# Kernel optimization log

Hardware: AMD Instinct MI355X
Metric: run time of the kernel (lower is better)

## Reference

```python
import jax, jax.numpy as jnp
import numpy as np

jax.config.update("jax_enable_x64", True)  # original uses torch fp64 for the reciprocal trick

# --- GenericE layout constants ---
N = 32            # NUM_POSITIONS
D = 128           # per-position feature dim
F = N * D         # flattened dim
B = 8192          # batch
NIB_A, NIB_B = 0, 1
SLOT_DIVIDEND, SLOT_DIVISOR, SLOT_REMAINDER, SLOT_QUOTIENT = 2, 3, 4, 5
OP_START, OPCODE, BASE = 64, 3, 2
S = 60.0          # DIV_SCALE
SM_S = 60.0       # SOFTMAX1_SCALE
OP_FLAT = 0 * D + OP_START + OPCODE  # flat index of opcode channel at position 0


def _build_weights():
    # ClearDivSlotsFFN: hidden_dim = 4 slots * 2 units; bake_clear_pair wiring
    cW_up = np.zeros((8, F), np.float32)
    cW_gate = np.zeros((8, F), np.float32)
    cW_down = np.zeros((F, 8), np.float32)
    for i, slot in enumerate([SLOT_DIVIDEND, SLOT_DIVISOR, SLOT_REMAINDER, SLOT_QUOTIENT]):
        h = 2 * i
        # delta[slot] = -(1/S) * relu(S*op_w) * slot_val  -> clears slot when opcode active
        cW_up[h, OP_FLAT] = S
        cW_gate[h, slot] = 1.0
        cW_down[slot, h] = -1.0 / S
        # guard unit of the pair (zero down weight, mirrors gather's guard unit)
        cW_up[h + 1, OP_FLAT] = -S
        cW_gate[h + 1, slot] = -1.0
    # GatherScalarFFN: hidden_dim = N + 1; wiring straight from the source
    H = N + 1
    gW_up = np.zeros((H, F), np.float32)
    gW_gate = np.zeros((H, F), np.float32)
    gW_down = np.zeros((F, H), np.float32)
    dst = 0 * D + SLOT_DIVIDEND
    for i in range(N):
        gW_up[i, OP_FLAT] = S
        gW_gate[i, i * D + NIB_A] = float(BASE ** i)
        gW_down[dst, i] = 1.0 / S
    gW_up[N, OP_FLAT] = -S
    gW_gate[N, dst] = -1.0
    # gW_down[dst, N] = 0.0 (explicit in source)
    return (jnp.asarray(cW_up), jnp.asarray(cW_gate), jnp.asarray(cW_down),
            jnp.asarray(gW_up), jnp.asarray(gW_gate), jnp.asarray(gW_down))


def setup_inputs() -> dict:
    key = jax.random.key(0)
    x = jax.random.uniform(key, (B, N, D), dtype=jnp.float32)
    cW_up, cW_gate, cW_down, gW_up, gW_gate, gW_down = _build_weights()
    base_powers = jnp.asarray([float(BASE ** j) for j in range(N)], dtype=jnp.float64)
    return {"x": x, "cW_up": cW_up, "cW_gate": cW_gate, "cW_down": cW_down,
            "gW_up": gW_up, "gW_gate": gW_gate, "gW_down": gW_down,
            "base_powers": base_powers}


def _ffn_delta(xf, W_up, W_gate, W_down):
    # GenericFlattenedFFN residual delta: W_down @ (relu(W_up x) * (W_gate x))
    h = jax.nn.relu(xf @ W_up.T) * (xf @ W_gate.T)   # [B, H]
    return h @ W_down.T                               # [B, F]


def reference(x, cW_up, cW_gate, cW_down, gW_up, gW_gate, gW_down, base_powers):
    Bc, Nc, Dc = x.shape
    xf = x.reshape(Bc, Nc * Dc)
    # d1 + d2: the two FFN branches (each branch's forward is x + delta, so diff is delta)
    d12 = _ffn_delta(xf, cW_up, cW_gate, cW_down) + _ffn_delta(xf, gW_up, gW_gate, gW_down)
    # d3: Softmax1 reciprocal trick in fp64 (matching torch .double())
    op_w = x[:, 0, OP_START + OPCODE]                         # [B]
    d = x[:, :Nc, NIB_B].astype(jnp.float64)                  # [B, N]
    val = jnp.maximum(d * base_powers, 0.5)
    scores = jnp.where(d > 0.5, jnp.log(val), jnp.float64(-SM_S))
    mx = scores.max(axis=-1, keepdims=True)                   # [B, 1]
    sum_ex = jnp.exp(scores - mx).sum(axis=-1)                # [B]
    recip = jnp.exp(-mx[..., 0]) / jnp.maximum(sum_ex, 1e-30)
    out = x + d12.reshape(Bc, Nc, Dc)
    return out.at[:, 0, SLOT_QUOTIENT].add(op_w * recip.astype(x.dtype))
```

## Files before the change

kernel.cpp:

```cpp
#include <hip/hip_runtime.h>
#include <math.h>


#define DDIM 128
#define FDIM 4096

__global__ __launch_bounds__(256) void div_merged_kernel(
    const float* __restrict__ x, float* __restrict__ out) {
  const long long row = blockIdx.x;
  const float* __restrict__ xr = x + row * (long long)FDIM;
  float* __restrict__ orow = out + row * (long long)FDIM;
  const int t = threadIdx.x;

  __shared__ float s_fix[4];

  if (t < 64) {
    const int lane = t;
    const bool active = lane < 32;
    double score = -60.0;
    double p = 0.0;
    if (active) {
      const double pw = (double)(1ULL << lane);
      const float va = xr[lane * DDIM + 0];
      const float vb = xr[lane * DDIM + 1];
      p = (double)va * pw;
      const double d = (double)vb;
      score = (d > 0.5) ? log(fmax(d * pw, 0.5)) : -60.0;
    }
    double mx = score;
#pragma unroll
    for (int off = 1; off < 64; off <<= 1)
      mx = fmax(mx, __shfl_xor(mx, off));
    double ex = active ? exp(score - mx) : 0.0;
#pragma unroll
    for (int off = 1; off < 64; off <<= 1) {
      ex += __shfl_xor(ex, off);
      p  += __shfl_xor(p, off);
    }
    if (lane == 0) {
      const float op    = xr[67];
      const float r60   = fmaxf(60.0f * op, 0.0f);
      const float inv60 = (float)(1.0 / 60.0);
      const double recip = exp(-mx) / fmax(ex, 1e-30);
      const float Pf = (float)p;
      const float x2 = xr[2], x3 = xr[3], x4v = xr[4], x5 = xr[5];
      const float dc2 = -((r60 * x2) * inv60);
      const float dc3 = -((r60 * x3) * inv60);
      const float dc4 = -((r60 * x4v) * inv60);
      const float dc5 = -((r60 * x5) * inv60);
      const float dg2 = (r60 * Pf) * inv60;
      s_fix[0] = x2 + (dc2 + dg2);
      s_fix[1] = x3 + dc3;
      s_fix[2] = x4v + dc4;
      s_fix[3] = (x5 + dc5) + op * (float)recip;
    }
  }
  __syncthreads();

  const float4* __restrict__ x4 = (const float4*)xr;
  float4* __restrict__ o4 = (float4*)orow;
#pragma unroll
  for (int k = 0; k < 4; ++k) {
    const int idx = k * 256 + t;
    float4 v = x4[idx];
    if (idx == 0) {
      v.z = s_fix[0];
      v.w = s_fix[1];
    } else if (idx == 1) {
      v.x = s_fix[2];
      v.y = s_fix[3];
    }
    o4[idx] = v;
  }
}

extern "C" void kernel_launch(void* const* d_in, const int* in_sizes, int n_in,
                              void* d_out, int out_size, void* d_ws, size_t ws_size,
                              hipStream_t stream) {
  const float* x = (const float*)d_in[0];
  float* out = (float*)d_out;
  const int rows = in_sizes[0] / FDIM;
  div_merged_kernel<<<rows, 256, 0, stream>>>(x, out);
}
```

Measured before the change: 244.0 us.

## Split per-row fixup into separate wave-per-row blocks, removing block barrier

The fixup work (softmax reciprocal over 32 positions and the slot updates) moves into dedicated blocks that each handle four rows, one wave per row. The bulk copy blocks no longer wait on a __syncthreads for that fixup and simply copy every float4 except the first two, which the fixup waves write. This is meant to remove the serialized fp64 reduction from the critical path of each copy block. In exchange it adds extra blocks, relies on rows being a multiple of 4, and has fixup waves rereading the row's first floats.

```diff
diff --git a/kernel.cpp b/kernel.cpp
--- a/kernel.cpp
+++ b/kernel.cpp
@@ -6,25 +6,26 @@
 #define FDIM 4096
 
 __global__ __launch_bounds__(256) void div_merged_kernel(
-    const float* __restrict__ x, float* __restrict__ out) {
-  const long long row = blockIdx.x;
-  const float* __restrict__ xr = x + row * (long long)FDIM;
-  float* __restrict__ orow = out + row * (long long)FDIM;
+    const float* __restrict__ x, float* __restrict__ out, int rows) {
+  const int bid = blockIdx.x;
   const int t = threadIdx.x;
+  const int nfix = rows >> 2;
 
-  __shared__ float s_fix[4];
+  if (bid < nfix) {
+    const int wave = t >> 6;
+    const int lane = t & 63;
+    const long long row = (long long)bid * 4 + wave;
+    const float* __restrict__ xr = x + row * (long long)FDIM;
+    float* __restrict__ orow = out + row * (long long)FDIM;
 
-  if (t < 64) {
-    const int lane = t;
     const bool active = lane < 32;
     double score = -60.0;
     double p = 0.0;
     if (active) {
+      const float2 ab = *(const float2*)(xr + lane * DDIM);
       const double pw = (double)(1ULL << lane);
-      const float va = xr[lane * DDIM + 0];
-      const float vb = xr[lane * DDIM + 1];
-      p = (double)va * pw;
-      const double d = (double)vb;
+      p = (double)ab.x * pw;
+      const double d = (double)ab.y;
       score = (d > 0.5) ? log(fmax(d * pw, 0.5)) : -60.0;
     }
     double mx = score;
@@ -43,34 +44,29 @@
       const float inv60 = (float)(1.0 / 60.0);
       const double recip = exp(-mx) / fmax(ex, 1e-30);
       const float Pf = (float)p;
-      const float x2 = xr[2], x3 = xr[3], x4v = xr[4], x5 = xr[5];
-      const float dc2 = -((r60 * x2) * inv60);
-      const float dc3 = -((r60 * x3) * inv60);
-      const float dc4 = -((r60 * x4v) * inv60);
-      const float dc5 = -((r60 * x5) * inv60);
+      float4 lo = *(const float4*)xr;
+      float4 hi = *(const float4*)(xr + 4);
+      const float dc2 = -((r60 * lo.z) * inv60);
+      const float dc3 = -((r60 * lo.w) * inv60);
+      const float dc4 = -((r60 * hi.x) * inv60);
+      const float dc5 = -((r60 * hi.y) * inv60);
       const float dg2 = (r60 * Pf) * inv60;
-      s_fix[0] = x2 + (dc2 + dg2);
-      s_fix[1] = x3 + dc3;
-      s_fix[2] = x4v + dc4;
-      s_fix[3] = (x5 + dc5) + op * (float)recip;
+      lo.z = lo.z + (dc2 + dg2);
+      lo.w = lo.w + dc3;
+      hi.x = hi.x + dc4;
+      hi.y = (hi.y + dc5) + op * (float)recip;
+      *(float4*)orow = lo;
+      *(float4*)(orow + 4) = hi;
     }
-  }
-  __syncthreads();
-
-  const float4* __restrict__ x4 = (const float4*)xr;
-  float4* __restrict__ o4 = (float4*)orow;
+  } else {
+    const long long row = bid - nfix;
+    const float4* __restrict__ x4 = (const float4*)(x + row * (long long)FDIM);
+    float4* __restrict__ o4 = (float4*)(out + row * (long long)FDIM);
 #pragma unroll
-  for (int k = 0; k < 4; ++k) {
-    const int idx = k * 256 + t;
-    float4 v = x4[idx];
-    if (idx == 0) {
-      v.z = s_fix[0];
-      v.w = s_fix[1];
-    } else if (idx == 1) {
-      v.x = s_fix[2];
-      v.y = s_fix[3];
+    for (int k = 0; k < 4; ++k) {
+      const int idx = k * 256 + t;
+      if (idx >= 2) o4[idx] = x4[idx];
     }
-    o4[idx] = v;
   }
 }
 
@@ -80,5 +76,6 @@
   const float* x = (const float*)d_in[0];
   float* out = (float*)d_out;
   const int rows = in_sizes[0] / FDIM;
-  div_merged_kernel<<<rows, 256, 0, stream>>>(x, out);
+  const int nfix = rows >> 2;
+  div_merged_kernel<<<rows + nfix, 256, 0, stream>>>(x, out, rows);
 }
```

After: 248.6 us. About the same (+1.9%).
